# Kernel tuning notes

Measured on AMD Instinct MI355X. Metric: run time of the kernel, lower is better.

## Reference

```python
import jax, jax.numpy as jnp
import numpy as np

D_MODEL = 1024
DK = 1024
DV = 1024
B, S = 8, 2048


def setup_inputs() -> dict:
    key = jax.random.key(0)
    ks = jax.random.split(key, 7)
    lim = 1.0 / np.sqrt(D_MODEL)
    x = jax.random.normal(ks[0], (B, S, D_MODEL), dtype=jnp.float32)
    Wq = jax.random.uniform(ks[1], (D_MODEL, DK), minval=-lim, maxval=lim, dtype=jnp.float32)
    bq = jax.random.uniform(ks[2], (DK,), minval=-lim, maxval=lim, dtype=jnp.float32)
    Wk = jax.random.uniform(ks[3], (D_MODEL, DK), minval=-lim, maxval=lim, dtype=jnp.float32)
    bk = jax.random.uniform(ks[4], (DK,), minval=-lim, maxval=lim, dtype=jnp.float32)
    Wv = jax.random.uniform(ks[5], (D_MODEL, DV), minval=-lim, maxval=lim, dtype=jnp.float32)
    bv = jax.random.uniform(ks[6], (DV,), minval=-lim, maxval=lim, dtype=jnp.float32)
    return {"x": x, "Wq": Wq, "bq": bq, "Wk": Wk, "bk": bk, "Wv": Wv, "bv": bv}


def reference(x, Wq, bq, Wk, bk, Wv, bv):
    # QKV projections: [B,S,d_model] -> [B,S,dk/dv]
    q = jnp.einsum('bsd,dk->bsk', x, Wq) + bq
    k = jnp.einsum('bsd,dk->bsk', x, Wk) + bk
    v = jnp.einsum('bsd,dv->bsv', x, Wv) + bv
    scale = 1.0 / jnp.sqrt(jnp.float32(DK))
    # scores: [B,S,S]
    scores = jnp.einsum('bqk,bsk->bqs', q, k) * scale
    probs = jax.nn.softmax(scores, axis=-1)
    return jnp.einsum('bqs,bsv->bqv', probs, v)
```

## Files before the change

kernel.cpp:

```cpp
#include <hip/hip_runtime.h>


#define DEV __device__ __forceinline__

typedef unsigned short u16;
typedef __attribute__((ext_vector_type(8))) short bf16x8;
typedef __attribute__((ext_vector_type(4))) float f32x4;

DEV float bf2f(u16 u) {
  unsigned v = ((unsigned)u) << 16;
  float f;
  __builtin_memcpy(&f, &v, 4);
  return f;
}
DEV u16 f2bf(float f) {
  unsigned v;
  __builtin_memcpy(&v, &f, 4);
  return (u16)((v + 0x7fffu + ((v >> 16) & 1u)) >> 16);
}

DEV void gload16(const u16* g, u16* l) {
  __builtin_amdgcn_global_load_lds(
      (const __attribute__((address_space(1))) void*)g,
      (__attribute__((address_space(3))) void*)l, 16, 0, 0);
}

#define BAR() __builtin_amdgcn_s_barrier()
#define SCHED0() __builtin_amdgcn_sched_barrier(0)
#define LGKM(n) asm volatile("s_waitcnt lgkmcnt(" #n ")" ::: "memory")
#define VMC6() asm volatile("s_waitcnt vmcnt(6)" ::: "memory")
#define VMC0() asm volatile("s_waitcnt vmcnt(0)" ::: "memory")

__global__ __launch_bounds__(256) void cvt_f32_bf16(const float* __restrict__ x,
                                                    u16* __restrict__ y) {
  const long long i = ((long long)blockIdx.x * 256 + threadIdx.x) * 4;
  float4 v = *(const float4*)&x[i];
  ushort4 o;
  o.x = f2bf(v.x); o.y = f2bf(v.y); o.z = f2bf(v.z); o.w = f2bf(v.w);
  *(ushort4*)&y[i] = o;
}

__global__ __launch_bounds__(256) void transpose_cvt3(
    const float* __restrict__ Wq, const float* __restrict__ Wk,
    const float* __restrict__ Wv, u16* __restrict__ Wt) {
  __shared__ float tl[64][65];
  const float* W = blockIdx.z == 0 ? Wq : blockIdx.z == 1 ? Wk : Wv;
  u16* dst = Wt + (long long)blockIdx.z * 1048576LL;
  const int n0 = blockIdx.x * 64;
  const int k0 = blockIdx.y * 64;
  const int tid = threadIdx.x;
  const int c = tid & 31, r = tid >> 5;
#pragma unroll
  for (int i = 0; i < 8; ++i) {
    const int k = i * 8 + r;
    float2 v2 = *(const float2*)&W[(long long)(k0 + k) * 1024 + n0 + c * 2];
    tl[k][c * 2] = v2.x;
    tl[k][c * 2 + 1] = v2.y;
  }
  __syncthreads();
#pragma unroll
  for (int i = 0; i < 8; ++i) {
    const int n = i * 8 + r;
    ushort2 o;
    o.x = f2bf(tl[c * 2][n]);
    o.y = f2bf(tl[c * 2 + 1][n]);
    *(ushort2*)&dst[(long long)(n0 + n) * 1024 + k0 + c * 2] = o;
  }
}

__global__ __launch_bounds__(256) void reduce_ml(const float* __restrict__ PS,
                                                 float* __restrict__ Li) {
  const int i = blockIdx.x * 256 + threadIdx.x;
  const int z = i >> 11, r = i & 2047;
  const float* ps = PS + ((long long)(z * 8) << 11) + r;
  float L = 0.f;
#pragma unroll
  for (int p = 0; p < 8; ++p) L += ps[p << 11];
  Li[i] = 1.0f / L;
}


template <int OUT_MODE>
__global__ __launch_bounds__(512, 2) void gemm256(
    const u16* __restrict__ A, const u16* __restrict__ B,
    const float* __restrict__ bias, void* __restrict__ Cv, int K, int lda,
    int ldb, int ldc, long long bA, long long bB, long long bC, float scale,
    const float* __restrict__ pm, float* __restrict__ ps) {
  __shared__ __attribute__((aligned(16))) char smem[131072];
  const int tid = threadIdx.x;
  const int w = tid >> 6, l = tid & 63;
  const int wr = w >> 2, wc = w & 3;

  const int gx = gridDim.x, gy = gridDim.y;
  long long flat =
      blockIdx.x + (long long)gx * (blockIdx.y + (long long)gy * blockIdx.z);
  const long long nwg = (long long)gx * gy * gridDim.z;
  if ((nwg & 7) == 0) flat = (flat & 7) * (nwg >> 3) + (flat >> 3);
  const int bx = (int)(flat % gx);
  const long long rem = flat / gx;
  const int by = (int)(rem % gy);
  const int z = (int)(rem / gy);

  A += (long long)z * bA;
  B += (long long)z * bB;
  const long long tm = (long long)by * 256;
  const long long tn = (long long)bx * 256;

  const int l15 = l & 15, hi4 = l >> 4, x7 = l & 7;
  const int slot0 = (hi4 ^ x7) * 16;
  const int slot1 = ((4 + hi4) ^ x7) * 16;
  const char* baseA0 = smem + (2 + wr) * 16384 + l15 * 128 + slot0;
  const char* baseA1 = smem + (2 + wr) * 16384 + l15 * 128 + slot1;
  const char* baseB0 = smem + (wc >> 1) * 16384 + ((wc & 1) * 64 + l15) * 128 + slot0;
  const char* baseB1 = smem + (wc >> 1) * 16384 + ((wc & 1) * 64 + l15) * 128 + slot1;

  const int lr = l >> 3;
  const long long scol = (long long)((x7 ^ lr) * 8);
  const u16* pBu0 = B + (tn + w * 16 + 0 + lr) * (long long)ldb + scol;
  const u16* pBu1 = B + (tn + w * 16 + 8 + lr) * (long long)ldb + scol;
  const u16* pBl0 = B + (tn + 128 + w * 16 + 0 + lr) * (long long)ldb + scol;
  const u16* pBl1 = B + (tn + 128 + w * 16 + 8 + lr) * (long long)ldb + scol;
  const u16* pAu0 = A + (tm + w * 16 + 0 + lr) * (long long)lda + scol;
  const u16* pAu1 = A + (tm + w * 16 + 8 + lr) * (long long)lda + scol;
  const u16* pAl0 = A + (tm + 128 + w * 16 + 0 + lr) * (long long)lda + scol;
  const u16* pAl1 = A + (tm + 128 + w * 16 + 8 + lr) * (long long)lda + scol;

#define STG(P0, P1, PART, BO)                                          \
  gload16(P0, (u16*)(smem + (BO) + (PART) * 16384 + (w * 2) * 1024));  \
  gload16(P1, (u16*)(smem + (BO) + (PART) * 16384 + (w * 2 + 1) * 1024)); \
  P0 += 64;                                                            \
  P1 += 64;

#define RDB(BO)                                                   \
  _Pragma("unroll") for (int ni = 0; ni < 4; ++ni) {              \
    bfrag[ni][0] = *(const bf16x8*)(baseB0 + (BO) + ni * 2048);   \
    bfrag[ni][1] = *(const bf16x8*)(baseB1 + (BO) + ni * 2048);   \
  }

#define RDP(DST, MLO, BO)                                         \
  DST[0][0] = *(const bf16x8*)(baseA0 + (BO) + (MLO)*2048);       \
  DST[0][1] = *(const bf16x8*)(baseA1 + (BO) + (MLO)*2048);       \
  DST[1][0] = *(const bf16x8*)(baseA0 + (BO) + (MLO + 1) * 2048); \
  DST[1][1] = *(const bf16x8*)(baseA1 + (BO) + (MLO + 1) * 2048);

#define MFMAP(AC0, AC1, AP)                                              \
  __builtin_amdgcn_s_setprio(1);                                         \
  _Pragma("unroll") for (int kk = 0; kk < 2; ++kk)                       \
      _Pragma("unroll") for (int ni = 0; ni < 4; ++ni) {                 \
    AC0[ni] = __builtin_amdgcn_mfma_f32_16x16x32_bf16(AP[0][kk],         \
                                                      bfrag[ni][kk],     \
                                                      AC0[ni], 0, 0, 0); \
    AC1[ni] = __builtin_amdgcn_mfma_f32_16x16x32_bf16(AP[1][kk],         \
                                                      bfrag[ni][kk],     \
                                                      AC1[ni], 0, 0, 0); \
  }                                                                      \
  __builtin_amdgcn_s_setprio(0);

#define KTILE(BO, OBO, T)                          \
  RDP(aB_, 2, BO);                                 \
  if ((T) + 1 < nt) { STG(pAl0, pAl1, 3, OBO); }   \
  BAR();                                           \
  LGKM(4);                                         \
  SCHED0();                                        \
  MFMAP(acc[0], acc[1], aA);                       \
  BAR();                                           \
  RDP(aA, 4, BO);                                  \
  if ((T) + 2 < nt) { STG(pBu0, pBu1, 0, BO); }    \
  BAR();                                           \
  LGKM(4);                                         \
  SCHED0();                                        \
  MFMAP(acc[2], acc[3], aB_);                      \
  BAR();                                           \
  RDP(aB_, 6, BO);                                 \
  if ((T) + 2 < nt) { STG(pBl0, pBl1, 1, BO); }    \
  BAR();                                           \
  LGKM(4);                                         \
  SCHED0();                                        \
  MFMAP(acc[4], acc[5], aA);                       \
  BAR();                                           \
  if ((T) + 2 < nt) {                              \
    STG(pAu0, pAu1, 2, BO);                        \
    VMC6();                                        \
  } else {                                         \
    VMC0();                                        \
  }                                                \
  BAR();                                           \
  if ((T) + 1 < nt) { RDP(aA, 0, OBO); }           \
  LGKM(4);                                         \
  SCHED0();                                        \
  MFMAP(acc[6], acc[7], aB_);                      \
  if ((T) + 1 < nt) { RDB(OBO); }                  \
  BAR();

  f32x4 acc[8][4];
  const f32x4 zero = {0.f, 0.f, 0.f, 0.f};
#pragma unroll
  for (int i = 0; i < 8; ++i)
#pragma unroll
    for (int j = 0; j < 4; ++j) acc[i][j] = zero;

  bf16x8 bfrag[4][2], aA[2][2], aB_[2][2];
  const int nt = K >> 6;

  STG(pBu0, pBu1, 0, 0);
  STG(pBl0, pBl1, 1, 0);
  STG(pAu0, pAu1, 2, 0);
  STG(pAl0, pAl1, 3, 0);
  STG(pBu0, pBu1, 0, 65536);
  STG(pBl0, pBl1, 1, 65536);
  STG(pAu0, pAu1, 2, 65536);
  VMC6();
  BAR();
  RDP(aA, 0, 0);
  RDB(0);

  for (int t = 0; t < nt; t += 2) {
    KTILE(0, 65536, t);
    KTILE(65536, 0, t + 1);
  }

  const int ro4 = (l >> 4) * 4;
  const int co = l & 15;
  if (OUT_MODE == 4) {
    float* C = (float*)Cv + (long long)z * bC;
#pragma unroll
    for (int mi = 0; mi < 8; ++mi) {
      const long long row0 = tm + wr * 128 + mi * 16 + ro4;
      float li[4];
#pragma unroll
      for (int r = 0; r < 4; ++r) li[r] = pm[(long long)z * 2048 + row0 + r];
#pragma unroll
      for (int ni = 0; ni < 4; ++ni) {
        const long long col = tn + wc * 64 + ni * 16 + co;
#pragma unroll
        for (int r = 0; r < 4; ++r)
          C[(row0 + r) * ldc + col] = acc[mi][ni][r] * li[r];
      }
    }
  } else if (OUT_MODE == 1) {
    u16* C = (u16*)Cv + (long long)z * bC;
    float* lps = (float*)smem;
#pragma unroll
    for (int mi = 0; mi < 8; ++mi) {
      const long long row0 = tm + wr * 128 + mi * 16 + ro4;
#pragma unroll
      for (int r = 0; r < 4; ++r) {
        float s_ = 0.f;
#pragma unroll
        for (int ni = 0; ni < 4; ++ni) {
          const float e = __builtin_amdgcn_exp2f(acc[mi][ni][r] * scale);
          s_ += e;
          C[(row0 + r) * ldc + tn + wc * 64 + ni * 16 + co] = f2bf(e);
        }
#pragma unroll
        for (int off = 1; off < 16; off <<= 1) s_ += __shfl_xor(s_, off, 64);
        if (co == 0) lps[(wr * 128 + mi * 16 + ro4 + r) * 4 + wc] = s_;
      }
    }
    __syncthreads();
    if (tid < 256) {
      const float S = lps[tid * 4] + lps[tid * 4 + 1] + lps[tid * 4 + 2] +
                      lps[tid * 4 + 3];
      ps[(((long long)z * 8 + bx) << 11) + tm + tid] = S;
    }
  } else {
    u16* C = (u16*)Cv + (long long)z * bC;
#pragma unroll
    for (int mi = 0; mi < 8; ++mi) {
      const long long row0 = tm + wr * 128 + mi * 16 + ro4;
#pragma unroll
      for (int ni = 0; ni < 4; ++ni) {
        const long long col = tn + wc * 64 + ni * 16 + co;
        const float badd = (OUT_MODE == 0) ? bias[col] : 0.f;
#pragma unroll
        for (int r = 0; r < 4; ++r) {
          float v = acc[mi][ni][r];
          if (OUT_MODE == 0) v += badd;
          if (OUT_MODE == 3) v += bias[row0 + r];
          C[(row0 + r) * ldc + col] = f2bf(v);
        }
      }
    }
  }
}

extern "C" void kernel_launch(void* const* d_in, const int* in_sizes, int n_in,
                              void* d_out, int out_size, void* d_ws,
                              size_t ws_size, hipStream_t stream) {
  const float* x = (const float*)d_in[0];
  const float* Wq = (const float*)d_in[1];
  const float* bq = (const float*)d_in[2];
  const float* Wk = (const float*)d_in[3];
  const float* bk = (const float*)d_in[4];
  const float* Wv = (const float*)d_in[5];
  const float* bv = (const float*)d_in[6];
  float* out = (float*)d_out;

  const long long MT = 16384LL;
  const long long D = 1024LL;

  u16* ws = (u16*)d_ws;
  u16* Wt = ws;
  u16* Q = Wt + 3 * 1048576LL;
  u16* Kb = Q + MT * D;
  u16* Vt = Kb + MT * D;
  u16* SC = Vt + MT * D;
  u16* xb = SC;
  float* PSa = (float*)d_ws;
  float* Li = PSa + 131072;

  const float cl2e = 1.4426950408889634f * 0.03125f;

  cvt_f32_bf16<<<dim3(16384), dim3(256), 0, stream>>>(x, xb);
  transpose_cvt3<<<dim3(16, 16, 3), dim3(256), 0, stream>>>(Wq, Wk, Wv, Wt);
  gemm256<0><<<dim3(4, 64, 1), dim3(512), 0, stream>>>(
      xb, Wt, bq, Q, 1024, 1024, 1024, 1024, 0, 0, 0, 0.f, nullptr, nullptr);
  gemm256<0><<<dim3(4, 64, 1), dim3(512), 0, stream>>>(
      xb, Wt + 1048576LL, bk, Kb, 1024, 1024, 1024, 1024, 0, 0, 0, 0.f,
      nullptr, nullptr);
  gemm256<3><<<dim3(64, 4, 1), dim3(512), 0, stream>>>(
      Wt + 2097152LL, xb, bv, Vt, 1024, 1024, 1024, 16384, 0, 0, 0, 0.f,
      nullptr, nullptr);
  gemm256<1><<<dim3(8, 8, 8), dim3(512), 0, stream>>>(
      Q, Kb, nullptr, SC, 1024, 1024, 1024, 2048, 2048 * 1024LL, 2048 * 1024LL,
      2048LL * 2048LL, cl2e, nullptr, PSa);
  reduce_ml<<<dim3(64), dim3(256), 0, stream>>>(PSa, Li);
  gemm256<4><<<dim3(4, 8, 8), dim3(512), 0, stream>>>(
      SC, Vt, nullptr, out, 2048, 2048, 16384, 1024, 2048LL * 2048LL, 2048LL,
      2048 * 1024LL, 0.f, Li, nullptr);
}
```

Measured before the change: 269.5 us.

## Fuse Q/K projections into one GEMM and double-buffer B fragments

The Q and K projection GEMMs are merged into a single launch that writes an interleaved QK buffer of width 2048, with a new output mode that picks bq or bk by column. The score GEMM now reads Q and K from that buffer with stride 2048. Inside the GEMM main loop, B fragments are double-buffered in registers (bfX/bfY) and loaded earlier. The loop is also split into full, penultimate and last tiles with tighter vmcnt waits and no branches in the steady state. The aim is to cut one launch, improve occupancy of the projection grid, and overlap LDS reads with MFMA. The cost is more register pressure and more fragile wait-count logic.

New measurement: 428.6 us. 1.59x slower.

```diff
diff --git a/kernel.cpp b/kernel.cpp
--- a/kernel.cpp
+++ b/kernel.cpp
@@ -28,8 +28,8 @@
 #define BAR() __builtin_amdgcn_s_barrier()
 #define SCHED0() __builtin_amdgcn_sched_barrier(0)
 #define LGKM(n) asm volatile("s_waitcnt lgkmcnt(" #n ")" ::: "memory")
-#define VMC6() asm volatile("s_waitcnt vmcnt(6)" ::: "memory")
-#define VMC0() asm volatile("s_waitcnt vmcnt(0)" ::: "memory")
+#define VMC(n) asm volatile("s_waitcnt vmcnt(" #n ")" ::: "memory")
+#define NOP
 
 __global__ __launch_bounds__(256) void cvt_f32_bf16(const float* __restrict__ x,
                                                     u16* __restrict__ y) {
@@ -131,10 +131,10 @@
   P0 += 64;                                                            \
   P1 += 64;
 
-#define RDB(BO)                                                   \
+#define RDB(BANK, BO)                                             \
   _Pragma("unroll") for (int ni = 0; ni < 4; ++ni) {              \
-    bfrag[ni][0] = *(const bf16x8*)(baseB0 + (BO) + ni * 2048);   \
-    bfrag[ni][1] = *(const bf16x8*)(baseB1 + (BO) + ni * 2048);   \
+    BANK[ni][0] = *(const bf16x8*)(baseB0 + (BO) + ni * 2048);    \
+    BANK[ni][1] = *(const bf16x8*)(baseB1 + (BO) + ni * 2048);    \
   }
 
 #define RDP(DST, MLO, BO)                                         \
@@ -143,54 +143,65 @@
   DST[1][0] = *(const bf16x8*)(baseA0 + (BO) + (MLO + 1) * 2048); \
   DST[1][1] = *(const bf16x8*)(baseA1 + (BO) + (MLO + 1) * 2048);
 
-#define MFMAP(AC0, AC1, AP)                                              \
+#define MFMAP(AC0, AC1, AP, BANK)                                        \
   __builtin_amdgcn_s_setprio(1);                                         \
   _Pragma("unroll") for (int kk = 0; kk < 2; ++kk)                       \
       _Pragma("unroll") for (int ni = 0; ni < 4; ++ni) {                 \
     AC0[ni] = __builtin_amdgcn_mfma_f32_16x16x32_bf16(AP[0][kk],         \
-                                                      bfrag[ni][kk],     \
+                                                      BANK[ni][kk],      \
                                                       AC0[ni], 0, 0, 0); \
     AC1[ni] = __builtin_amdgcn_mfma_f32_16x16x32_bf16(AP[1][kk],         \
-                                                      bfrag[ni][kk],     \
+                                                      BANK[ni][kk],      \
                                                       AC1[ni], 0, 0, 0); \
   }                                                                      \
   __builtin_amdgcn_s_setprio(0);
 
-#define KTILE(BO, OBO, T)                          \
-  RDP(aB_, 2, BO);                                 \
-  if ((T) + 1 < nt) { STG(pAl0, pAl1, 3, OBO); }   \
-  BAR();                                           \
-  LGKM(4);                                         \
-  SCHED0();                                        \
-  MFMAP(acc[0], acc[1], aA);                       \
-  BAR();                                           \
-  RDP(aA, 4, BO);                                  \
-  if ((T) + 2 < nt) { STG(pBu0, pBu1, 0, BO); }    \
-  BAR();                                           \
-  LGKM(4);                                         \
-  SCHED0();                                        \
-  MFMAP(acc[2], acc[3], aB_);                      \
-  BAR();                                           \
-  RDP(aB_, 6, BO);                                 \
-  if ((T) + 2 < nt) { STG(pBl0, pBl1, 1, BO); }    \
-  BAR();                                           \
-  LGKM(4);                                         \
-  SCHED0();                                        \
-  MFMAP(acc[4], acc[5], aA);                       \
-  BAR();                                           \
-  if ((T) + 2 < nt) {                              \
-    STG(pAu0, pAu1, 2, BO);                        \
-    VMC6();                                        \
-  } else {                                         \
-    VMC0();                                        \
-  }                                                \
-  BAR();                                           \
-  if ((T) + 1 < nt) { RDP(aA, 0, OBO); }           \
-  LGKM(4);                                         \
-  SCHED0();                                        \
-  MFMAP(acc[6], acc[7], aB_);                      \
-  if ((T) + 1 < nt) { RDB(OBO); }                  \
+#define KTILE_GEN(BO, OBO, BF, BFN, S0, S1, S2, S3, W1, W2, W3, W4, NEXT) \
+  RDP(aB_, 2, BO);                                                        \
+  S0;                                                                     \
+  BAR();                                                                  \
+  LGKM(4);                                                                \
+  SCHED0();                                                               \
+  MFMAP(acc[0], acc[1], aA, BF);                                          \
+  BAR();                                                                  \
+  RDP(aA, 4, BO);                                                         \
+  S1;                                                                     \
+  W1;                                                                     \
+  BAR();                                                                  \
+  LGKM(4);                                                                \
+  SCHED0();                                                               \
+  MFMAP(acc[2], acc[3], aB_, BF);                                         \
+  BAR();                                                                  \
+  RDP(aB_, 6, BO);                                                        \
+  S2;                                                                     \
+  W2;                                                                     \
+  BAR();                                                                  \
+  LGKM(4);                                                                \
+  SCHED0();                                                               \
+  MFMAP(acc[4], acc[5], aA, BF);                                          \
+  SCHED0();                                                               \
+  if (NEXT) { RDB(BFN, OBO); }                                            \
+  BAR();                                                                  \
+  S3;                                                                     \
+  W3;                                                                     \
+  BAR();                                                                  \
+  SCHED0();                                                               \
+  if (NEXT) { RDP(aA, 0, OBO); }                                          \
+  W4;                                                                     \
+  SCHED0();                                                               \
+  MFMAP(acc[6], acc[7], aB_, BF);                                         \
   BAR();
+
+#define KT_FULL(BO, OBO, BF, BFN)                                         \
+  KTILE_GEN(BO, OBO, BF, BFN, STG(pAl0, pAl1, 3, OBO),                    \
+            STG(pBu0, pBu1, 0, BO), STG(pBl0, pBl1, 1, BO),               \
+            STG(pAu0, pAu1, 2, BO), VMC(8), VMC(8), VMC(6), LGKM(12), 1)
+#define KT_PEN(BO, OBO, BF, BFN)                                          \
+  KTILE_GEN(BO, OBO, BF, BFN, STG(pAl0, pAl1, 3, OBO), NOP, NOP, NOP,     \
+            VMC(6), VMC(4), VMC(0), LGKM(12), 1)
+#define KT_LAST(BO, OBO, BF, BFN)                                         \
+  KTILE_GEN(BO, OBO, BF, BFN, NOP, NOP, NOP, NOP, NOP, NOP, NOP,          \
+            LGKM(0), 0)
 
   f32x4 acc[8][4];
   const f32x4 zero = {0.f, 0.f, 0.f, 0.f};
@@ -199,7 +210,7 @@
 #pragma unroll
     for (int j = 0; j < 4; ++j) acc[i][j] = zero;
 
-  bf16x8 bfrag[4][2], aA[2][2], aB_[2][2];
+  bf16x8 bfX[4][2], bfY[4][2], aA[2][2], aB_[2][2];
   const int nt = K >> 6;
 
   STG(pBu0, pBu1, 0, 0);
@@ -209,15 +220,18 @@
   STG(pBu0, pBu1, 0, 65536);
   STG(pBl0, pBl1, 1, 65536);
   STG(pAu0, pAu1, 2, 65536);
-  VMC6();
+  VMC(6);
   BAR();
+  SCHED0();
   RDP(aA, 0, 0);
-  RDB(0);
-
-  for (int t = 0; t < nt; t += 2) {
-    KTILE(0, 65536, t);
-    KTILE(65536, 0, t + 1);
-  }
+  RDB(bfX, 0);
+
+  for (int t = 0; t < nt - 2; t += 2) {
+    KT_FULL(0, 65536, bfX, bfY);
+    KT_FULL(65536, 0, bfY, bfX);
+  }
+  KT_PEN(0, 65536, bfX, bfY);
+  KT_LAST(65536, 0, bfY, bfX);
 
   const int ro4 = (l >> 4) * 4;
   const int co = l & 15;
@@ -271,11 +285,14 @@
 #pragma unroll
       for (int ni = 0; ni < 4; ++ni) {
         const long long col = tn + wc * 64 + ni * 16 + co;
-        const float badd = (OUT_MODE == 0) ? bias[col] : 0.f;
+        float badd = 0.f;
+        if (OUT_MODE == 0) badd = bias[col];
+        if (OUT_MODE == 5)
+          badd = (col < 1024) ? bias[col] : pm[col - 1024];
 #pragma unroll
         for (int r = 0; r < 4; ++r) {
           float v = acc[mi][ni][r];
-          if (OUT_MODE == 0) v += badd;
+          if (OUT_MODE == 0 || OUT_MODE == 5) v += badd;
           if (OUT_MODE == 3) v += bias[row0 + r];
           C[(row0 + r) * ldc + col] = f2bf(v);
         }
@@ -301,9 +318,8 @@
 
   u16* ws = (u16*)d_ws;
   u16* Wt = ws;
-  u16* Q = Wt + 3 * 1048576LL;
-  u16* Kb = Q + MT * D;
-  u16* Vt = Kb + MT * D;
+  u16* QK = Wt + 3 * 1048576LL;
+  u16* Vt = QK + MT * 2048LL;
   u16* SC = Vt + MT * D;
   u16* xb = SC;
   float* PSa = (float*)d_ws;
@@ -313,17 +329,14 @@
 
   cvt_f32_bf16<<<dim3(16384), dim3(256), 0, stream>>>(x, xb);
   transpose_cvt3<<<dim3(16, 16, 3), dim3(256), 0, stream>>>(Wq, Wk, Wv, Wt);
-  gemm256<0><<<dim3(4, 64, 1), dim3(512), 0, stream>>>(
-      xb, Wt, bq, Q, 1024, 1024, 1024, 1024, 0, 0, 0, 0.f, nullptr, nullptr);
-  gemm256<0><<<dim3(4, 64, 1), dim3(512), 0, stream>>>(
-      xb, Wt + 1048576LL, bk, Kb, 1024, 1024, 1024, 1024, 0, 0, 0, 0.f,
-      nullptr, nullptr);
+  gemm256<5><<<dim3(8, 64, 1), dim3(512), 0, stream>>>(
+      xb, Wt, bq, QK, 1024, 1024, 1024, 2048, 0, 0, 0, 0.f, bk, nullptr);
   gemm256<3><<<dim3(64, 4, 1), dim3(512), 0, stream>>>(
       Wt + 2097152LL, xb, bv, Vt, 1024, 1024, 1024, 16384, 0, 0, 0, 0.f,
       nullptr, nullptr);
   gemm256<1><<<dim3(8, 8, 8), dim3(512), 0, stream>>>(
-      Q, Kb, nullptr, SC, 1024, 1024, 1024, 2048, 2048 * 1024LL, 2048 * 1024LL,
-      2048LL * 2048LL, cl2e, nullptr, PSa);
+      QK, QK + 1024, nullptr, SC, 1024, 2048, 2048, 2048, 2048 * 2048LL,
+      2048 * 2048LL, 2048LL * 2048LL, cl2e, nullptr, PSa);
   reduce_ml<<<dim3(64), dim3(256), 0, stream>>>(PSa, Li);
   gemm256<4><<<dim3(4, 8, 8), dim3(512), 0, stream>>>(
       SC, Vt, nullptr, out, 2048, 2048, 16384, 1024, 2048LL * 2048LL, 2048LL,
```

## Replace 256x256 GEMM tile with 128x256 tile, K-step 32, higher occupancy

Applied to the files above, without the earlier changes.

The GEMM kernel tile shrinks from 256x256 to 128x256 with a K step of 32. LDS drops from 128KB to 48KB, the launch bound targets 4 blocks per CU, and the grids double. The finely interleaved multi-phase prefetch schedule is replaced by a simpler double-buffered loop: load fragments, barrier, issue the next stage, run 16 MFMAs. The goal is more resident waves and more blocks to hide latency. The cost is lower arithmetic intensity per tile and barriers every 32-wide K step.

Result: slower. 299.5 us (+11.1%).

```diff
diff --git a/kernel.cpp b/kernel.cpp
--- a/kernel.cpp
+++ b/kernel.cpp
@@ -27,9 +27,8 @@
 
 #define BAR() __builtin_amdgcn_s_barrier()
 #define SCHED0() __builtin_amdgcn_sched_barrier(0)
-#define LGKM(n) asm volatile("s_waitcnt lgkmcnt(" #n ")" ::: "memory")
-#define VMC6() asm volatile("s_waitcnt vmcnt(6)" ::: "memory")
-#define VMC0() asm volatile("s_waitcnt vmcnt(0)" ::: "memory")
+#define LGKM0() asm volatile("s_waitcnt lgkmcnt(0)" ::: "memory")
+#define VMC(n) asm volatile("s_waitcnt vmcnt(" #n ")" ::: "memory")
 
 __global__ __launch_bounds__(256) void cvt_f32_bf16(const float* __restrict__ x,
                                                     u16* __restrict__ y) {
@@ -81,12 +80,12 @@
 
 
 template <int OUT_MODE>
-__global__ __launch_bounds__(512, 2) void gemm256(
+__global__ __launch_bounds__(512, 4) void gemm128(
     const u16* __restrict__ A, const u16* __restrict__ B,
     const float* __restrict__ bias, void* __restrict__ Cv, int K, int lda,
     int ldb, int ldc, long long bA, long long bB, long long bC, float scale,
     const float* __restrict__ pm, float* __restrict__ ps) {
-  __shared__ __attribute__((aligned(16))) char smem[131072];
+  __shared__ __attribute__((aligned(16))) char smem[49152];
   const int tid = threadIdx.x;
   const int w = tid >> 6, l = tid & 63;
   const int wr = w >> 2, wc = w & 3;
@@ -103,120 +102,77 @@
 
   A += (long long)z * bA;
   B += (long long)z * bB;
-  const long long tm = (long long)by * 256;
+  const long long tm = (long long)by * 128;
   const long long tn = (long long)bx * 256;
 
-  const int l15 = l & 15, hi4 = l >> 4, x7 = l & 7;
-  const int slot0 = (hi4 ^ x7) * 16;
-  const int slot1 = ((4 + hi4) ^ x7) * 16;
-  const char* baseA0 = smem + (2 + wr) * 16384 + l15 * 128 + slot0;
-  const char* baseA1 = smem + (2 + wr) * 16384 + l15 * 128 + slot1;
-  const char* baseB0 = smem + (wc >> 1) * 16384 + ((wc & 1) * 64 + l15) * 128 + slot0;
-  const char* baseB1 = smem + (wc >> 1) * 16384 + ((wc & 1) * 64 + l15) * 128 + slot1;
-
-  const int lr = l >> 3;
-  const long long scol = (long long)((x7 ^ lr) * 8);
-  const u16* pBu0 = B + (tn + w * 16 + 0 + lr) * (long long)ldb + scol;
-  const u16* pBu1 = B + (tn + w * 16 + 8 + lr) * (long long)ldb + scol;
-  const u16* pBl0 = B + (tn + 128 + w * 16 + 0 + lr) * (long long)ldb + scol;
-  const u16* pBl1 = B + (tn + 128 + w * 16 + 8 + lr) * (long long)ldb + scol;
-  const u16* pAu0 = A + (tm + w * 16 + 0 + lr) * (long long)lda + scol;
-  const u16* pAu1 = A + (tm + w * 16 + 8 + lr) * (long long)lda + scol;
-  const u16* pAl0 = A + (tm + 128 + w * 16 + 0 + lr) * (long long)lda + scol;
-  const u16* pAl1 = A + (tm + 128 + w * 16 + 8 + lr) * (long long)lda + scol;
-
-#define STG(P0, P1, PART, BO)                                          \
-  gload16(P0, (u16*)(smem + (BO) + (PART) * 16384 + (w * 2) * 1024));  \
-  gload16(P1, (u16*)(smem + (BO) + (PART) * 16384 + (w * 2 + 1) * 1024)); \
-  P0 += 64;                                                            \
-  P1 += 64;
-
-#define RDB(BO)                                                   \
-  _Pragma("unroll") for (int ni = 0; ni < 4; ++ni) {              \
-    bfrag[ni][0] = *(const bf16x8*)(baseB0 + (BO) + ni * 2048);   \
-    bfrag[ni][1] = *(const bf16x8*)(baseB1 + (BO) + ni * 2048);   \
-  }
-
-#define RDP(DST, MLO, BO)                                         \
-  DST[0][0] = *(const bf16x8*)(baseA0 + (BO) + (MLO)*2048);       \
-  DST[0][1] = *(const bf16x8*)(baseA1 + (BO) + (MLO)*2048);       \
-  DST[1][0] = *(const bf16x8*)(baseA0 + (BO) + (MLO + 1) * 2048); \
-  DST[1][1] = *(const bf16x8*)(baseA1 + (BO) + (MLO + 1) * 2048);
-
-#define MFMAP(AC0, AC1, AP)                                              \
+  const int l15 = l & 15, hi4 = l >> 4;
+  const int slotc = (hi4 ^ ((l15 >> 1) & 3)) * 16;
+  const char* bA0 = smem + (wr * 64 + l15) * 64 + slotc;
+  const char* bB0 = smem + 8192 + (wc * 64 + l15) * 64 + slotc;
+
+  const int srow = tid >> 2;
+  const int kseg = (tid & 3) ^ ((tid >> 3) & 3);
+  const int tid16 = tid * 16;
+  const u16* pA = A + (tm + srow) * (long long)lda + kseg * 8;
+  const u16* pB0 = B + (tn + srow) * (long long)ldb + kseg * 8;
+  const u16* pB1 = B + (tn + 128 + srow) * (long long)ldb + kseg * 8;
+
+#define STG(BO)                                           \
+  gload16(pA, (u16*)(smem + (BO) + tid16));               \
+  gload16(pB0, (u16*)(smem + (BO) + 8192 + tid16));       \
+  gload16(pB1, (u16*)(smem + (BO) + 16384 + tid16));      \
+  pA += 32;                                               \
+  pB0 += 32;                                              \
+  pB1 += 32;
+
+#define RDAB(BO)                                                    \
+  _Pragma("unroll") for (int mi = 0; mi < 4; ++mi)                  \
+      afr[mi] = *(const bf16x8*)(bA0 + (BO) + mi * 1024);           \
+  _Pragma("unroll") for (int ni = 0; ni < 4; ++ni)                  \
+      bfr[ni] = *(const bf16x8*)(bB0 + (BO) + ni * 1024);
+
+#define MFMAT()                                                          \
   __builtin_amdgcn_s_setprio(1);                                         \
-  _Pragma("unroll") for (int kk = 0; kk < 2; ++kk)                       \
-      _Pragma("unroll") for (int ni = 0; ni < 4; ++ni) {                 \
-    AC0[ni] = __builtin_amdgcn_mfma_f32_16x16x32_bf16(AP[0][kk],         \
-                                                      bfrag[ni][kk],     \
-                                                      AC0[ni], 0, 0, 0); \
-    AC1[ni] = __builtin_amdgcn_mfma_f32_16x16x32_bf16(AP[1][kk],         \
-                                                      bfrag[ni][kk],     \
-                                                      AC1[ni], 0, 0, 0); \
-  }                                                                      \
+  _Pragma("unroll") for (int ni = 0; ni < 4; ++ni)                       \
+      _Pragma("unroll") for (int mi = 0; mi < 4; ++mi)                   \
+          acc[mi][ni] = __builtin_amdgcn_mfma_f32_16x16x32_bf16(         \
+              afr[mi], bfr[ni], acc[mi][ni], 0, 0, 0);                   \
   __builtin_amdgcn_s_setprio(0);
 
-#define KTILE(BO, OBO, T)                          \
-  RDP(aB_, 2, BO);                                 \
-  if ((T) + 1 < nt) { STG(pAl0, pAl1, 3, OBO); }   \
-  BAR();                                           \
-  LGKM(4);                                         \
-  SCHED0();                                        \
-  MFMAP(acc[0], acc[1], aA);                       \
-  BAR();                                           \
-  RDP(aA, 4, BO);                                  \
-  if ((T) + 2 < nt) { STG(pBu0, pBu1, 0, BO); }    \
-  BAR();                                           \
-  LGKM(4);                                         \
-  SCHED0();                                        \
-  MFMAP(acc[2], acc[3], aB_);                      \
-  BAR();                                           \
-  RDP(aB_, 6, BO);                                 \
-  if ((T) + 2 < nt) { STG(pBl0, pBl1, 1, BO); }    \
-  BAR();                                           \
-  LGKM(4);                                         \
-  SCHED0();                                        \
-  MFMAP(acc[4], acc[5], aA);                       \
-  BAR();                                           \
-  if ((T) + 2 < nt) {                              \
-    STG(pAu0, pAu1, 2, BO);                        \
-    VMC6();                                        \
-  } else {                                         \
-    VMC0();                                        \
-  }                                                \
-  BAR();                                           \
-  if ((T) + 1 < nt) { RDP(aA, 0, OBO); }           \
-  LGKM(4);                                         \
-  SCHED0();                                        \
-  MFMAP(acc[6], acc[7], aB_);                      \
-  if ((T) + 1 < nt) { RDB(OBO); }                  \
+#define TILE(BO, T)                  \
+  RDAB(BO);                          \
+  LGKM0();                           \
+  SCHED0();                          \
+  BAR();                             \
+  if ((T) + 2 < nt) {                \
+    STG(BO);                         \
+    VMC(3);                          \
+  } else {                           \
+    VMC(0);                          \
+  }                                  \
+  SCHED0();                          \
+  MFMAT();                           \
+  SCHED0();                          \
   BAR();
 
-  f32x4 acc[8][4];
+  f32x4 acc[4][4];
   const f32x4 zero = {0.f, 0.f, 0.f, 0.f};
 #pragma unroll
-  for (int i = 0; i < 8; ++i)
+  for (int i = 0; i < 4; ++i)
 #pragma unroll
     for (int j = 0; j < 4; ++j) acc[i][j] = zero;
 
-  bf16x8 bfrag[4][2], aA[2][2], aB_[2][2];
-  const int nt = K >> 6;
-
-  STG(pBu0, pBu1, 0, 0);
-  STG(pBl0, pBl1, 1, 0);
-  STG(pAu0, pAu1, 2, 0);
-  STG(pAl0, pAl1, 3, 0);
-  STG(pBu0, pBu1, 0, 65536);
-  STG(pBl0, pBl1, 1, 65536);
-  STG(pAu0, pAu1, 2, 65536);
-  VMC6();
+  bf16x8 afr[4], bfr[4];
+  const int nt = K >> 5;
+
+  STG(0);
+  STG(24576);
+  VMC(3);
   BAR();
-  RDP(aA, 0, 0);
-  RDB(0);
 
   for (int t = 0; t < nt; t += 2) {
-    KTILE(0, 65536, t);
-    KTILE(65536, 0, t + 1);
+    TILE(0, t);
+    TILE(24576, t + 1);
   }
 
   const int ro4 = (l >> 4) * 4;
@@ -224,8 +180,8 @@
   if (OUT_MODE == 4) {
     float* C = (float*)Cv + (long long)z * bC;
 #pragma unroll
-    for (int mi = 0; mi < 8; ++mi) {
-      const long long row0 = tm + wr * 128 + mi * 16 + ro4;
+    for (int mi = 0; mi < 4; ++mi) {
+      const long long row0 = tm + wr * 64 + mi * 16 + ro4;
       float li[4];
 #pragma unroll
       for (int r = 0; r < 4; ++r) li[r] = pm[(long long)z * 2048 + row0 + r];
@@ -241,8 +197,8 @@
     u16* C = (u16*)Cv + (long long)z * bC;
     float* lps = (float*)smem;
 #pragma unroll
-    for (int mi = 0; mi < 8; ++mi) {
-      const long long row0 = tm + wr * 128 + mi * 16 + ro4;
+    for (int mi = 0; mi < 4; ++mi) {
+      const long long row0 = tm + wr * 64 + mi * 16 + ro4;
 #pragma unroll
       for (int r = 0; r < 4; ++r) {
         float s_ = 0.f;
@@ -254,11 +210,11 @@
         }
 #pragma unroll
         for (int off = 1; off < 16; off <<= 1) s_ += __shfl_xor(s_, off, 64);
-        if (co == 0) lps[(wr * 128 + mi * 16 + ro4 + r) * 4 + wc] = s_;
+        if (co == 0) lps[(wr * 64 + mi * 16 + ro4 + r) * 4 + wc] = s_;
       }
     }
     __syncthreads();
-    if (tid < 256) {
+    if (tid < 128) {
       const float S = lps[tid * 4] + lps[tid * 4 + 1] + lps[tid * 4 + 2] +
                       lps[tid * 4 + 3];
       ps[(((long long)z * 8 + bx) << 11) + tm + tid] = S;
@@ -266,8 +222,8 @@
   } else {
     u16* C = (u16*)Cv + (long long)z * bC;
 #pragma unroll
-    for (int mi = 0; mi < 8; ++mi) {
-      const long long row0 = tm + wr * 128 + mi * 16 + ro4;
+    for (int mi = 0; mi < 4; ++mi) {
+      const long long row0 = tm + wr * 64 + mi * 16 + ro4;
 #pragma unroll
       for (int ni = 0; ni < 4; ++ni) {
         const long long col = tn + wc * 64 + ni * 16 + co;
@@ -313,19 +269,19 @@
 
   cvt_f32_bf16<<<dim3(16384), dim3(256), 0, stream>>>(x, xb);
   transpose_cvt3<<<dim3(16, 16, 3), dim3(256), 0, stream>>>(Wq, Wk, Wv, Wt);
-  gemm256<0><<<dim3(4, 64, 1), dim3(512), 0, stream>>>(
+  gemm128<0><<<dim3(4, 128, 1), dim3(512), 0, stream>>>(
       xb, Wt, bq, Q, 1024, 1024, 1024, 1024, 0, 0, 0, 0.f, nullptr, nullptr);
-  gemm256<0><<<dim3(4, 64, 1), dim3(512), 0, stream>>>(
+  gemm128<0><<<dim3(4, 128, 1), dim3(512), 0, stream>>>(
       xb, Wt + 1048576LL, bk, Kb, 1024, 1024, 1024, 1024, 0, 0, 0, 0.f,
       nullptr, nullptr);
-  gemm256<3><<<dim3(64, 4, 1), dim3(512), 0, stream>>>(
+  gemm128<3><<<dim3(64, 8, 1), dim3(512), 0, stream>>>(
       Wt + 2097152LL, xb, bv, Vt, 1024, 1024, 1024, 16384, 0, 0, 0, 0.f,
       nullptr, nullptr);
-  gemm256<1><<<dim3(8, 8, 8), dim3(512), 0, stream>>>(
+  gemm128<1><<<dim3(8, 16, 8), dim3(512), 0, stream>>>(
       Q, Kb, nullptr, SC, 1024, 1024, 1024, 2048, 2048 * 1024LL, 2048 * 1024LL,
       2048LL * 2048LL, cl2e, nullptr, PSa);
   reduce_ml<<<dim3(64), dim3(256), 0, stream>>>(PSa, Li);
-  gemm256<4><<<dim3(4, 8, 8), dim3(512), 0, stream>>>(
+  gemm128<4><<<dim3(4, 16, 8), dim3(512), 0, stream>>>(
       SC, Vt, nullptr, out, 2048, 2048, 16384, 1024, 2048LL * 2048LL, 2048LL,
       2048 * 1024LL, 0.f, Li, nullptr);
 }
```

## Switch GEMM to 32x32x16 MFMA fragments and merge prep kernels

Applied to the files above, without the earlier changes.

The GEMM inner loop moves from 16x16x32 bf16 MFMA to 32x32x16 MFMA, which changes the LDS fragment read pattern, accumulator layout and all epilogue index mappings. Larger MFMA tiles give more FLOPs per instruction and fewer LDS reads per flop. The input conversion and weight transpose kernels are also fused into a single launch to save one kernel launch. The risk is that the new lane-to-row mapping in the epilogues must match the 32x32 output layout exactly, and the stores become less contiguous.

New measurement: 303.5 us. 1.13x slower.

```diff
diff --git a/kernel.cpp b/kernel.cpp
--- a/kernel.cpp
+++ b/kernel.cpp
@@ -5,7 +5,7 @@
 
 typedef unsigned short u16;
 typedef __attribute__((ext_vector_type(8))) short bf16x8;
-typedef __attribute__((ext_vector_type(4))) float f32x4;
+typedef __attribute__((ext_vector_type(16))) float f32x16;
 
 DEV float bf2f(u16 u) {
   unsigned v = ((unsigned)u) << 16;
@@ -31,24 +31,27 @@
 #define VMC6() asm volatile("s_waitcnt vmcnt(6)" ::: "memory")
 #define VMC0() asm volatile("s_waitcnt vmcnt(0)" ::: "memory")
 
-__global__ __launch_bounds__(256) void cvt_f32_bf16(const float* __restrict__ x,
-                                                    u16* __restrict__ y) {
-  const long long i = ((long long)blockIdx.x * 256 + threadIdx.x) * 4;
-  float4 v = *(const float4*)&x[i];
-  ushort4 o;
-  o.x = f2bf(v.x); o.y = f2bf(v.y); o.z = f2bf(v.z); o.w = f2bf(v.w);
-  *(ushort4*)&y[i] = o;
-}
-
-__global__ __launch_bounds__(256) void transpose_cvt3(
-    const float* __restrict__ Wq, const float* __restrict__ Wk,
-    const float* __restrict__ Wv, u16* __restrict__ Wt) {
+__global__ __launch_bounds__(256) void prep(const float* __restrict__ x,
+                                            const float* __restrict__ Wq,
+                                            const float* __restrict__ Wk,
+                                            const float* __restrict__ Wv,
+                                            u16* __restrict__ xb,
+                                            u16* __restrict__ Wt) {
   __shared__ float tl[64][65];
-  const float* W = blockIdx.z == 0 ? Wq : blockIdx.z == 1 ? Wk : Wv;
-  u16* dst = Wt + (long long)blockIdx.z * 1048576LL;
-  const int n0 = blockIdx.x * 64;
-  const int k0 = blockIdx.y * 64;
   const int tid = threadIdx.x;
+  if (blockIdx.x < 16384) {
+    const long long i = ((long long)blockIdx.x * 256 + tid) * 4;
+    float4 v = *(const float4*)&x[i];
+    ushort4 o;
+    o.x = f2bf(v.x); o.y = f2bf(v.y); o.z = f2bf(v.z); o.w = f2bf(v.w);
+    *(ushort4*)&xb[i] = o;
+    return;
+  }
+  const int b = blockIdx.x - 16384;
+  const int bz = b >> 8, byk = (b >> 4) & 15, bxn = b & 15;
+  const float* W = bz == 0 ? Wq : bz == 1 ? Wk : Wv;
+  u16* dst = Wt + (long long)bz * 1048576LL;
+  const int n0 = bxn * 64, k0 = byk * 64;
   const int c = tid & 31, r = tid >> 5;
 #pragma unroll
   for (int i = 0; i < 8; ++i) {
@@ -106,16 +109,16 @@
   const long long tm = (long long)by * 256;
   const long long tn = (long long)bx * 256;
 
-  const int l15 = l & 15, hi4 = l >> 4, x7 = l & 7;
-  const int slot0 = (hi4 ^ x7) * 16;
-  const int slot1 = ((4 + hi4) ^ x7) * 16;
-  const char* baseA0 = smem + (2 + wr) * 16384 + l15 * 128 + slot0;
-  const char* baseA1 = smem + (2 + wr) * 16384 + l15 * 128 + slot1;
-  const char* baseB0 = smem + (wc >> 1) * 16384 + ((wc & 1) * 64 + l15) * 128 + slot0;
-  const char* baseB1 = smem + (wc >> 1) * 16384 + ((wc & 1) * 64 + l15) * 128 + slot1;
+  const int l31 = l & 31, h = l >> 5, x7 = l31 & 7;
+  const int sl0 = ((0 + h) ^ x7) * 16;
+  const int sl1 = ((2 + h) ^ x7) * 16;
+  const int sl2 = ((4 + h) ^ x7) * 16;
+  const int sl3 = ((6 + h) ^ x7) * 16;
+  const char* bAr = smem + (2 + wr) * 16384 + l31 * 128;
+  const char* bBr = smem + (wc >> 1) * 16384 + ((wc & 1) * 64 + l31) * 128;
 
   const int lr = l >> 3;
-  const long long scol = (long long)((x7 ^ lr) * 8);
+  const long long scol = (long long)(((l & 7) ^ lr) * 8);
   const u16* pBu0 = B + (tn + w * 16 + 0 + lr) * (long long)ldb + scol;
   const u16* pBu1 = B + (tn + w * 16 + 8 + lr) * (long long)ldb + scol;
   const u16* pBl0 = B + (tn + 128 + w * 16 + 0 + lr) * (long long)ldb + scol;
@@ -131,52 +134,49 @@
   P0 += 64;                                                            \
   P1 += 64;
 
-#define RDB(BO)                                                   \
-  _Pragma("unroll") for (int ni = 0; ni < 4; ++ni) {              \
-    bfrag[ni][0] = *(const bf16x8*)(baseB0 + (BO) + ni * 2048);   \
-    bfrag[ni][1] = *(const bf16x8*)(baseB1 + (BO) + ni * 2048);   \
-  }
-
-#define RDP(DST, MLO, BO)                                         \
-  DST[0][0] = *(const bf16x8*)(baseA0 + (BO) + (MLO)*2048);       \
-  DST[0][1] = *(const bf16x8*)(baseA1 + (BO) + (MLO)*2048);       \
-  DST[1][0] = *(const bf16x8*)(baseA0 + (BO) + (MLO + 1) * 2048); \
-  DST[1][1] = *(const bf16x8*)(baseA1 + (BO) + (MLO + 1) * 2048);
-
-#define MFMAP(AC0, AC1, AP)                                              \
+#define RDB(BO)                                                      \
+  _Pragma("unroll") for (int ni = 0; ni < 2; ++ni) {                 \
+    bfrag[ni][0] = *(const bf16x8*)(bBr + (BO) + ni * 4096 + sl0);   \
+    bfrag[ni][1] = *(const bf16x8*)(bBr + (BO) + ni * 4096 + sl1);   \
+    bfrag[ni][2] = *(const bf16x8*)(bBr + (BO) + ni * 4096 + sl2);   \
+    bfrag[ni][3] = *(const bf16x8*)(bBr + (BO) + ni * 4096 + sl3);   \
+  }
+
+#define RDF(DST, FR, BO)                                  \
+  DST[0] = *(const bf16x8*)(bAr + (BO) + (FR)*4096 + sl0); \
+  DST[1] = *(const bf16x8*)(bAr + (BO) + (FR)*4096 + sl1); \
+  DST[2] = *(const bf16x8*)(bAr + (BO) + (FR)*4096 + sl2); \
+  DST[3] = *(const bf16x8*)(bAr + (BO) + (FR)*4096 + sl3);
+
+#define MFMAF(ACR, AP)                                                   \
   __builtin_amdgcn_s_setprio(1);                                         \
-  _Pragma("unroll") for (int kk = 0; kk < 2; ++kk)                       \
-      _Pragma("unroll") for (int ni = 0; ni < 4; ++ni) {                 \
-    AC0[ni] = __builtin_amdgcn_mfma_f32_16x16x32_bf16(AP[0][kk],         \
-                                                      bfrag[ni][kk],     \
-                                                      AC0[ni], 0, 0, 0); \
-    AC1[ni] = __builtin_amdgcn_mfma_f32_16x16x32_bf16(AP[1][kk],         \
-                                                      bfrag[ni][kk],     \
-                                                      AC1[ni], 0, 0, 0); \
-  }                                                                      \
+  _Pragma("unroll") for (int kk = 0; kk < 4; ++kk)                       \
+      _Pragma("unroll") for (int ni = 0; ni < 2; ++ni)                   \
+          ACR[ni] = __builtin_amdgcn_mfma_f32_32x32x16_bf16(             \
+              AP[kk], bfrag[ni][kk], ACR[ni], 0, 0, 0);                  \
   __builtin_amdgcn_s_setprio(0);
 
 #define KTILE(BO, OBO, T)                          \
-  RDP(aB_, 2, BO);                                 \
+  RDF(aB_, 1, BO);                                 \
   if ((T) + 1 < nt) { STG(pAl0, pAl1, 3, OBO); }   \
   BAR();                                           \
   LGKM(4);                                         \
   SCHED0();                                        \
-  MFMAP(acc[0], acc[1], aA);                       \
-  BAR();                                           \
-  RDP(aA, 4, BO);                                  \
+  MFMAF(acc[0], aA);                               \
+  BAR();                                           \
+  RDF(aA, 2, BO);                                  \
   if ((T) + 2 < nt) { STG(pBu0, pBu1, 0, BO); }    \
   BAR();                                           \
   LGKM(4);                                         \
   SCHED0();                                        \
-  MFMAP(acc[2], acc[3], aB_);                      \
-  BAR();                                           \
-  RDP(aB_, 6, BO);                                 \
+  MFMAF(acc[1], aB_);                              \
+  BAR();                                           \
+  RDF(aB_, 3, BO);                                 \
   if ((T) + 2 < nt) { STG(pBl0, pBl1, 1, BO); }    \
   BAR();                                           \
   LGKM(4);                                         \
   SCHED0();                                        \
-  MFMAP(acc[4], acc[5], aA);                       \
+  MFMAF(acc[2], aA);                               \
   BAR();                                           \
   if ((T) + 2 < nt) {                              \
     STG(pAu0, pAu1, 2, BO);                        \
@@ -185,21 +185,22 @@
     VMC0();                                        \
   }                                                \
   BAR();                                           \
-  if ((T) + 1 < nt) { RDP(aA, 0, OBO); }           \
+  if ((T) + 1 < nt) { RDF(aA, 0, OBO); }           \
   LGKM(4);                                         \
   SCHED0();                                        \
-  MFMAP(acc[6], acc[7], aB_);                      \
+  MFMAF(acc[3], aB_);                              \
   if ((T) + 1 < nt) { RDB(OBO); }                  \
   BAR();
 
-  f32x4 acc[8][4];
-  const f32x4 zero = {0.f, 0.f, 0.f, 0.f};
-#pragma unroll
-  for (int i = 0; i < 8; ++i)
-#pragma unroll
-    for (int j = 0; j < 4; ++j) acc[i][j] = zero;
-
-  bf16x8 bfrag[4][2], aA[2][2], aB_[2][2];
+  f32x16 acc[4][2];
+#pragma unroll
+  for (int i = 0; i < 4; ++i)
+#pragma unroll
+    for (int j = 0; j < 2; ++j)
+#pragma unroll
+      for (int e = 0; e < 16; ++e) acc[i][j][e] = 0.f;
+
+  bf16x8 bfrag[2][4], aA[4], aB_[4];
   const int nt = K >> 6;
 
   STG(pBu0, pBu1, 0, 0);
@@ -211,7 +212,7 @@
   STG(pAu0, pAu1, 2, 65536);
   VMC6();
   BAR();
-  RDP(aA, 0, 0);
+  RDF(aA, 0, 0);
   RDB(0);
 
   for (int t = 0; t < nt; t += 2) {
@@ -219,42 +220,46 @@
     KTILE(65536, 0, t + 1);
   }
 
-  const int ro4 = (l >> 4) * 4;
-  const int co = l & 15;
   if (OUT_MODE == 4) {
     float* C = (float*)Cv + (long long)z * bC;
 #pragma unroll
-    for (int mi = 0; mi < 8; ++mi) {
-      const long long row0 = tm + wr * 128 + mi * 16 + ro4;
-      float li[4];
-#pragma unroll
-      for (int r = 0; r < 4; ++r) li[r] = pm[(long long)z * 2048 + row0 + r];
-#pragma unroll
-      for (int ni = 0; ni < 4; ++ni) {
-        const long long col = tn + wc * 64 + ni * 16 + co;
-#pragma unroll
-        for (int r = 0; r < 4; ++r)
-          C[(row0 + r) * ldc + col] = acc[mi][ni][r] * li[r];
+    for (int fr = 0; fr < 4; ++fr) {
+      const long long rb = tm + wr * 128 + fr * 32;
+      float lir[16];
+#pragma unroll
+      for (int rg = 0; rg < 16; ++rg)
+        lir[rg] =
+            pm[(long long)z * 2048 + rb + (rg & 3) + 8 * (rg >> 2) + 4 * h];
+#pragma unroll
+      for (int ni = 0; ni < 2; ++ni) {
+        const long long col = tn + wc * 64 + ni * 32 + l31;
+#pragma unroll
+        for (int rg = 0; rg < 16; ++rg) {
+          const long long row = rb + (rg & 3) + 8 * (rg >> 2) + 4 * h;
+          C[row * ldc + col] = acc[fr][ni][rg] * lir[rg];
+        }
       }
     }
   } else if (OUT_MODE == 1) {
     u16* C = (u16*)Cv + (long long)z * bC;
     float* lps = (float*)smem;
 #pragma unroll
-    for (int mi = 0; mi < 8; ++mi) {
-      const long long row0 = tm + wr * 128 + mi * 16 + ro4;
-#pragma unroll
-      for (int r = 0; r < 4; ++r) {
+    for (int fr = 0; fr < 4; ++fr) {
+      const long long rb = tm + wr * 128 + fr * 32;
+#pragma unroll
+      for (int rg = 0; rg < 16; ++rg) {
+        const int rloc = (rg & 3) + 8 * (rg >> 2) + 4 * h;
+        const long long row = rb + rloc;
         float s_ = 0.f;
 #pragma unroll
-        for (int ni = 0; ni < 4; ++ni) {
-          const float e = __builtin_amdgcn_exp2f(acc[mi][ni][r] * scale);
+        for (int ni = 0; ni < 2; ++ni) {
+          const float e = __builtin_amdgcn_exp2f(acc[fr][ni][rg] * scale);
           s_ += e;
-          C[(row0 + r) * ldc + tn + wc * 64 + ni * 16 + co] = f2bf(e);
+          C[row * ldc + tn + wc * 64 + ni * 32 + l31] = f2bf(e);
         }
 #pragma unroll
-        for (int off = 1; off < 16; off <<= 1) s_ += __shfl_xor(s_, off, 64);
-        if (co == 0) lps[(wr * 128 + mi * 16 + ro4 + r) * 4 + wc] = s_;
+        for (int off = 1; off < 32; off <<= 1) s_ += __shfl_xor(s_, off, 64);
+        if (l31 == 0) lps[(wr * 128 + fr * 32 + rloc) * 4 + wc] = s_;
       }
     }
     __syncthreads();
@@ -263,21 +268,35 @@
                       lps[tid * 4 + 3];
       ps[(((long long)z * 8 + bx) << 11) + tm + tid] = S;
     }
+  } else if (OUT_MODE == 0) {
+    u16* C = (u16*)Cv + (long long)z * bC;
+#pragma unroll
+    for (int fr = 0; fr < 4; ++fr) {
+      const long long rb = tm + wr * 128 + fr * 32;
+#pragma unroll
+      for (int ni = 0; ni < 2; ++ni) {
+        const long long col = tn + wc * 64 + ni * 32 + l31;
+        const float badd = bias[col];
+#pragma unroll
+        for (int rg = 0; rg < 16; ++rg) {
+          const long long row = rb + (rg & 3) + 8 * (rg >> 2) + 4 * h;
+          C[row * ldc + col] = f2bf(acc[fr][ni][rg] + badd);
+        }
+      }
+    }
   } else {
     u16* C = (u16*)Cv + (long long)z * bC;
 #pragma unroll
-    for (int mi = 0; mi < 8; ++mi) {
-      const long long row0 = tm + wr * 128 + mi * 16 + ro4;
-#pragma unroll
-      for (int ni = 0; ni < 4; ++ni) {
-        const long long col = tn + wc * 64 + ni * 16 + co;
-        const float badd = (OUT_MODE == 0) ? bias[col] : 0.f;
-#pragma unroll
-        for (int r = 0; r < 4; ++r) {
-          float v = acc[mi][ni][r];
-          if (OUT_MODE == 0) v += badd;
-          if (OUT_MODE == 3) v += bias[row0 + r];
-          C[(row0 + r) * ldc + col] = f2bf(v);
+    for (int fr = 0; fr < 4; ++fr) {
+      const long long rb = tm + wr * 128 + fr * 32;
+#pragma unroll
+      for (int rg = 0; rg < 16; ++rg) {
+        const long long row = rb + (rg & 3) + 8 * (rg >> 2) + 4 * h;
+        const float badd = bias[row];
+#pragma unroll
+        for (int ni = 0; ni < 2; ++ni) {
+          const long long col = tn + wc * 64 + ni * 32 + l31;
+          C[row * ldc + col] = f2bf(acc[fr][ni][rg] + badd);
         }
       }
     }
@@ -311,8 +330,7 @@
 
   const float cl2e = 1.4426950408889634f * 0.03125f;
 
-  cvt_f32_bf16<<<dim3(16384), dim3(256), 0, stream>>>(x, xb);
-  transpose_cvt3<<<dim3(16, 16, 3), dim3(256), 0, stream>>>(Wq, Wk, Wv, Wt);
+  prep<<<dim3(16384 + 768), dim3(256), 0, stream>>>(x, Wq, Wk, Wv, xb, Wt);
   gemm256<0><<<dim3(4, 64, 1), dim3(512), 0, stream>>>(
       xb, Wt, bq, Q, 1024, 1024, 1024, 1024, 0, 0, 0, 0.f, nullptr, nullptr);
   gemm256<0><<<dim3(4, 64, 1), dim3(512), 0, stream>>>(
```
